# Kernel tuning notes

Hardware: AMD Instinct MI355X
Metric: run time of the kernel (lower is better)

## Reference

```python
import jax, jax.numpy as jnp
import numpy as np

N_NODES = 50000
N_EDGES = 1600000
N_FEAT = 128
DIM = 128
N_GRAPHS = 128
BN_EPS = 1e-5


def setup_inputs() -> dict:
    key = jax.random.key(0)
    ks = jax.random.split(key, 16)
    x = jax.random.normal(ks[0], (N_NODES, N_FEAT), dtype=jnp.float32)
    edge_index = jax.random.randint(ks[1], (2, N_EDGES), 0, N_NODES)
    batch = jnp.sort(jax.random.randint(ks[2], (N_NODES,), 0, N_GRAPHS))
    def lin(k, fin, fout):
        return jax.random.normal(k, (fin, fout), dtype=jnp.float32) / np.sqrt(fin).astype(np.float32)
    inp = {"x": x, "edge_index": edge_index, "batch": batch}
    fins = [N_FEAT, DIM, DIM]
    for i in range(3):
        inp[f"W{i}"] = lin(ks[3 + i], fins[i], DIM)
        inp[f"b{i}"] = jnp.zeros((DIM,), jnp.float32)
        inp[f"g{i}"] = jnp.ones((DIM,), jnp.float32)
        inp[f"be{i}"] = jnp.zeros((DIM,), jnp.float32)
    return inp


def _gcn_norm(edge_index, n):
    # add self loops, symmetric normalization D^-1/2 (A+I) D^-1/2
    loop = jnp.arange(n, dtype=edge_index.dtype)
    src = jnp.concatenate([edge_index[0], loop])
    dst = jnp.concatenate([edge_index[1], loop])
    deg = jax.ops.segment_sum(jnp.ones_like(src, dtype=jnp.float32), dst, num_segments=n)
    dinv = jnp.where(deg > 0, jax.lax.rsqrt(deg), 0.0)
    norm = dinv[src] * dinv[dst]  # [E+N]
    return src, dst, norm


def _gcn_conv(h, W, b, src, dst, norm, n):
    h = h @ W                      # [N, D]
    msg = h[src] * norm[:, None]   # [E+N, D] gather + scale
    agg = jax.ops.segment_sum(msg, dst, num_segments=n)
    return agg + b


def _batchnorm(h, g, be):
    mu = jnp.mean(h, axis=0)
    var = jnp.mean(jnp.square(h - mu), axis=0)  # biased, training-mode BN
    return (h - mu) * jax.lax.rsqrt(var + BN_EPS) * g + be


def reference(x, edge_index, batch, W0, b0, g0, be0, W1, b1, g1, be1, W2, b2, g2, be2):
    n = x.shape[0]
    src, dst, norm = _gcn_norm(edge_index, n)
    params = [(W0, b0, g0, be0), (W1, b1, g1, be1), (W2, b2, g2, be2)]
    h = x
    pools = []
    for (W, b, g, be) in params:
        h = jax.nn.relu(_gcn_conv(h, W, b, src, dst, norm, n))
        h = _batchnorm(h, g, be)
        pools.append(jax.ops.segment_sum(h, batch, num_segments=N_GRAPHS))
    return jnp.concatenate(pools, axis=1)  # [N_GRAPHS, 3*DIM]
```

## Files before the change

### kernel.cpp

```cpp
#include <hip/hip_runtime.h>
#include <hip/hip_bf16.h>

#define N_GRAPHS 128
#define BN_EPS 1e-5f
#define CHUNK 8192
#define NBU 512
#define CAP 8192

typedef short bf16x8 __attribute__((ext_vector_type(8)));
typedef short s16x4 __attribute__((ext_vector_type(4)));
typedef float f32x4 __attribute__((ext_vector_type(4)));

__device__ __forceinline__ unsigned short f2b(float f) {
    unsigned int u = __builtin_bit_cast(unsigned int, f);
    u += 0x7FFFu + ((u >> 16) & 1u);
    return (unsigned short)(u >> 16);
}
__device__ __forceinline__ float b2f_lo(unsigned int p) {
    return __builtin_bit_cast(float, p << 16);
}
__device__ __forceinline__ float b2f_hi(unsigned int p) {
    return __builtin_bit_cast(float, p & 0xFFFF0000u);
}

__global__ __launch_bounds__(512) void bin_chunks(const int* __restrict__ src,
                                                  const int* __restrict__ dst,
                                                  unsigned int* __restrict__ bpairs,
                                                  int* __restrict__ cnts,
                                                  int* __restrict__ cbase,
                                                  int* __restrict__ btot, int E) {
    __shared__ int lhist[NBU], lscan[NBU], lfill[NBU];
    int tid = threadIdx.x;
    int c0 = blockIdx.x * CHUNK;
    int ecnt = min(CHUNK, E - c0);
    lhist[tid] = 0;
    __syncthreads();
    for (int i = tid; i < ecnt; i += 512)
        atomicAdd(&lhist[((unsigned)dst[c0 + i]) >> 7], 1);
    __syncthreads();
    int orig = lhist[tid];
    atomicAdd(&btot[tid], orig);
    lscan[tid] = orig;
    __syncthreads();
    for (int off = 1; off < NBU; off <<= 1) {
        int t = (tid >= off) ? lscan[tid - off] : 0;
        __syncthreads();
        lscan[tid] += t;
        __syncthreads();
    }
    int excl = lscan[tid] - orig;
    cnts[blockIdx.x * NBU + tid] = orig;
    cbase[blockIdx.x * NBU + tid] = excl;
    lfill[tid] = 0;
    __syncthreads();
    lscan[tid] = excl;
    __syncthreads();
    for (int i = tid; i < ecnt; i += 512) {
        int d = dst[c0 + i], s = src[c0 + i];
        int b = ((unsigned)d) >> 7;
        int pos = lscan[b] + atomicAdd(&lfill[b], 1);
        bpairs[c0 + pos] = ((unsigned)(d & 127) << 25) | (unsigned)s;
    }
}

__global__ __launch_bounds__(512) void bucket_scan(const int* __restrict__ btot,
                                                   int* __restrict__ bucket_base) {
    __shared__ int s[NBU];
    int b = threadIdx.x;
    int tot = btot[b];
    s[b] = tot;
    __syncthreads();
    for (int off = 1; off < NBU; off <<= 1) {
        int t = (b >= off) ? s[b - off] : 0;
        __syncthreads();
        s[b] += t;
        __syncthreads();
    }
    bucket_base[b] = s[b] - tot;
}

__global__ __launch_bounds__(256) void bucket_csr(const unsigned int* __restrict__ bpairs,
                                                  const int* __restrict__ cnts,
                                                  const int* __restrict__ cbase,
                                                  const int* __restrict__ bucket_base,
                                                  int* __restrict__ rowp,
                                                  int* __restrict__ degarr,
                                                  float* __restrict__ dinv,
                                                  int* __restrict__ csr,
                                                  int nchunks, int N) {
    __shared__ unsigned int lpr[CAP];
    __shared__ int lcsr[CAP];
    __shared__ int ccnt[256], cofs[256], cb[256];
    __shared__ int lhist[128], lofs[128], lfill[128];
    int tid = threadIdx.x;
    int b = blockIdx.x;
    int bb = bucket_base[b];
    int total = bucket_base[b + 1] - bb;
    if (total > CAP) total = CAP;

    ccnt[tid] = (tid < nchunks) ? cnts[tid * NBU + b] : 0;
    cb[tid]   = (tid < nchunks) ? cbase[tid * NBU + b] : 0;
    cofs[tid] = ccnt[tid];
    __syncthreads();
    int orig = cofs[tid];
    for (int off = 1; off < 256; off <<= 1) {
        int t = (tid >= off) ? cofs[tid - off] : 0;
        __syncthreads();
        cofs[tid] += t;
        __syncthreads();
    }
    int o = cofs[tid] - orig;
    if (tid < nchunks) {
        int len = ccnt[tid];
        const unsigned int* p = bpairs + (size_t)tid * CHUNK + cb[tid];
        for (int i = 0; i < len; ++i) {
            int q = o + i;
            if (q < CAP) lpr[q] = p[i];
        }
    }
    if (tid < 128) { lhist[tid] = 0; lfill[tid] = 0; }
    __syncthreads();
    for (int i = tid; i < total; i += 256)
        atomicAdd(&lhist[lpr[i] >> 25], 1);
    __syncthreads();
    if (tid < 128) lofs[tid] = lhist[tid];
    __syncthreads();
    for (int off = 1; off < 128; off <<= 1) {
        int t = 0;
        if (tid < 128 && tid >= off) t = lofs[tid - off];
        __syncthreads();
        if (tid < 128) lofs[tid] += t;
        __syncthreads();
    }
    if (tid < 128) {
        int v = b * 128 + tid;
        if (v < N) {
            int dg = lhist[tid];
            degarr[v] = dg;
            rowp[v] = bb + lofs[tid] - dg;
            dinv[v] = rsqrtf((float)(dg + 1));
        }
    }
    __syncthreads();
    for (int i = tid; i < total; i += 256) {
        unsigned int pr = lpr[i];
        int dl = pr >> 25;
        int pos = lofs[dl] - lhist[dl] + atomicAdd(&lfill[dl], 1);
        if (pos < CAP) lcsr[pos] = (int)(pr & 0x1FFFFFFu);
    }
    __syncthreads();
    for (int i = tid; i < total; i += 256) csr[bb + i] = lcsr[i];
}

__global__ __launch_bounds__(256) void prep_w(const float* __restrict__ W,
                                              const float* __restrict__ sc,
                                              unsigned short* __restrict__ Wp) {
    int i = blockIdx.x * 256 + threadIdx.x;
    int k = i >> 7, c = i & 127;
    float w = W[i];
    if (sc) w *= sc[k];
    int kk = k & 31, k0 = k >> 5;
    int hi = (kk >> 2) & 3;
    int e = (kk & 3) + 4 * (kk >> 4);
    int idx = c * 128 + k0 * 32 + hi * 8 + e;
    Wp[idx ^ ((c & 7) << 3)] = f2b(w);
}

template <int AF32>
__global__ __launch_bounds__(256) void gemm_mfma(const void* __restrict__ Avoid,
                                                 const unsigned short* __restrict__ Wp,
                                                 const float* __restrict__ wb,
                                                 const float* __restrict__ dinv,
                                                 unsigned short* __restrict__ Cb, int N) {
    __shared__ unsigned short sWt[128 * 128];
    int tid = threadIdx.x;
    {
        const uint4* src = (const uint4*)Wp;
        uint4* dst = (uint4*)sWt;
#pragma unroll
        for (int j = 0; j < 8; ++j) dst[tid + 256 * j] = src[tid + 256 * j];
    }
    __syncthreads();

    int wave = tid >> 6, lane = tid & 63;
    int lo4 = lane & 15, hi = lane >> 4;
    int rowBase = blockIdx.x * 128 + wave * 32;

    f32x4 acc[8][2];
#pragma unroll
    for (int ct = 0; ct < 8; ++ct)
#pragma unroll
        for (int rt = 0; rt < 2; ++rt) acc[ct][rt] = (f32x4){0.f, 0.f, 0.f, 0.f};

    const float* Af = (const float*)Avoid;
    const unsigned short* Ab = (const unsigned short*)Avoid;

    for (int k0 = 0; k0 < 128; k0 += 32) {
        bf16x8 bfrag[2];
#pragma unroll
        for (int rt = 0; rt < 2; ++rt) {
            int r = rowBase + rt * 16 + lo4;
            if (r >= N) r = N - 1;
            if (AF32) {
                float4 f0 = *(const float4*)(Af + (size_t)r * 128 + k0 + 4 * hi);
                float4 f1 = *(const float4*)(Af + (size_t)r * 128 + k0 + 16 + 4 * hi);
                bf16x8 f;
                f[0] = (short)f2b(f0.x); f[1] = (short)f2b(f0.y);
                f[2] = (short)f2b(f0.z); f[3] = (short)f2b(f0.w);
                f[4] = (short)f2b(f1.x); f[5] = (short)f2b(f1.y);
                f[6] = (short)f2b(f1.z); f[7] = (short)f2b(f1.w);
                bfrag[rt] = f;
            } else {
                s16x4 a0 = *(const s16x4*)(Ab + (size_t)r * 128 + k0 + 4 * hi);
                s16x4 a1 = *(const s16x4*)(Ab + (size_t)r * 128 + k0 + 16 + 4 * hi);
                bf16x8 f;
                f[0] = a0[0]; f[1] = a0[1]; f[2] = a0[2]; f[3] = a0[3];
                f[4] = a1[0]; f[5] = a1[1]; f[6] = a1[2]; f[7] = a1[3];
                bfrag[rt] = f;
            }
        }
        int kq = k0 >> 5;
#pragma unroll
        for (int ct = 0; ct < 8; ++ct) {
            int c = ct * 16 + lo4;
            int idx = (c * 128 + kq * 32 + hi * 8) ^ ((c & 7) << 3);
            bf16x8 af = *(const bf16x8*)(sWt + idx);
#pragma unroll
            for (int rt = 0; rt < 2; ++rt)
                acc[ct][rt] = __builtin_amdgcn_mfma_f32_16x16x32_bf16(af, bfrag[rt], acc[ct][rt], 0, 0, 0);
        }
    }

#pragma unroll
    for (int rt = 0; rt < 2; ++rt) {
        int r = rowBase + rt * 16 + lo4;
        if (r < N) {
            float dv = dinv[r];
#pragma unroll
            for (int ct = 0; ct < 8; ++ct) {
                int c0 = ct * 16 + hi * 4;
                float4 wbv = make_float4(0.f, 0.f, 0.f, 0.f);
                if (!AF32) wbv = *(const float4*)(wb + c0);
                ushort4 s;
                s.x = f2b((acc[ct][rt][0] + wbv.x) * dv);
                s.y = f2b((acc[ct][rt][1] + wbv.y) * dv);
                s.z = f2b((acc[ct][rt][2] + wbv.z) * dv);
                s.w = f2b((acc[ct][rt][3] + wbv.w) * dv);
                *(ushort4*)(Cb + (size_t)r * 128 + c0) = s;
            }
        }
    }
}

__global__ __launch_bounds__(256) void agg_relu_b16(const unsigned int* __restrict__ hW32,
                                                    const int* __restrict__ rowp,
                                                    const int* __restrict__ cnt,
                                                    const int* __restrict__ csr,
                                                    const float* __restrict__ dinv,
                                                    const float* __restrict__ bias,
                                                    unsigned int* __restrict__ z32, int N) {
    int wave = threadIdx.x >> 6, lane = threadIdx.x & 63;
    int v = blockIdx.x * 4 + wave;
    if (v >= N) return;
    int beg = rowp[v];
    int num = cnt[v];
    float s0 = 0.f, s1 = 0.f;
    int i = 0;
    for (; i + 4 <= num; i += 4) {
        int u0 = csr[beg + i + 0];
        int u1 = csr[beg + i + 1];
        int u2 = csr[beg + i + 2];
        int u3 = csr[beg + i + 3];
        unsigned int p0 = hW32[(size_t)u0 * 64 + lane];
        unsigned int p1 = hW32[(size_t)u1 * 64 + lane];
        unsigned int p2 = hW32[(size_t)u2 * 64 + lane];
        unsigned int p3 = hW32[(size_t)u3 * 64 + lane];
        s0 += b2f_lo(p0) + b2f_lo(p1) + b2f_lo(p2) + b2f_lo(p3);
        s1 += b2f_hi(p0) + b2f_hi(p1) + b2f_hi(p2) + b2f_hi(p3);
    }
    for (; i < num; ++i) {
        int u = csr[beg + i];
        unsigned int p = hW32[(size_t)u * 64 + lane];
        s0 += b2f_lo(p);
        s1 += b2f_hi(p);
    }
    float dv = dinv[v];
    unsigned int pv = hW32[(size_t)v * 64 + lane];
    float r0 = dv * (s0 + b2f_lo(pv)) + bias[2 * lane];
    float r1 = dv * (s1 + b2f_hi(pv)) + bias[2 * lane + 1];
    unsigned int po = (unsigned int)f2b(fmaxf(r0, 0.f)) | ((unsigned int)f2b(fmaxf(r1, 0.f)) << 16);
    z32[(size_t)v * 64 + lane] = po;
}

__global__ __launch_bounds__(256) void bn_stats_b16(const unsigned int* __restrict__ z32,
                                                    float* __restrict__ stats, int N) {
    int lane = threadIdx.x & 63, sub = threadIdx.x >> 6;
    float s0 = 0.f, s1 = 0.f, q0 = 0.f, q1 = 0.f;
    for (int v = blockIdx.x * 4 + sub; v < N; v += gridDim.x * 4) {
        unsigned int p = z32[(size_t)v * 64 + lane];
        float a = b2f_lo(p), c = b2f_hi(p);
        s0 += a; q0 = fmaf(a, a, q0);
        s1 += c; q1 = fmaf(c, c, q1);
    }
    __shared__ float ls[256][4];
    ls[threadIdx.x][0] = s0; ls[threadIdx.x][1] = s1;
    ls[threadIdx.x][2] = q0; ls[threadIdx.x][3] = q1;
    __syncthreads();
    if (sub == 0) {
        for (int k = 1; k < 4; ++k) {
            s0 += ls[lane + 64 * k][0]; s1 += ls[lane + 64 * k][1];
            q0 += ls[lane + 64 * k][2]; q1 += ls[lane + 64 * k][3];
        }
        atomicAdd(&stats[2 * lane], s0);
        atomicAdd(&stats[2 * lane + 1], s1);
        atomicAdd(&stats[128 + 2 * lane], q0);
        atomicAdd(&stats[129 + 2 * lane], q1);
    }
}

__global__ void bn_finalize_wb(const float* __restrict__ stats, const float* __restrict__ g,
                               const float* __restrict__ be, float* __restrict__ ss,
                               const float* __restrict__ Wnext, float* __restrict__ wb,
                               float invN) {
    __shared__ float shv[128];
    int d = threadIdx.x;
    float mu = stats[d] * invN;
    float var = stats[128 + d] * invN - mu * mu;
    float sc = g[d] * rsqrtf(var + BN_EPS);
    float sh = be[d] - mu * sc;
    ss[d] = sc;
    ss[128 + d] = sh;
    shv[d] = sh;
    __syncthreads();
    if (Wnext) {
        float acc = 0.f;
#pragma unroll 4
        for (int k = 0; k < 128; ++k) acc = fmaf(shv[k], Wnext[k * 128 + d], acc);
        wb[d] = acc;
    }
}

__global__ __launch_bounds__(64) void apply_pool_b16(const unsigned int* __restrict__ z32,
                                                     const float* __restrict__ ss,
                                                     const int* __restrict__ batch,
                                                     float* __restrict__ out,
                                                     int layer, int N) {
    __shared__ int gb[32];
    int lane = threadIdx.x;
    int v0 = blockIdx.x * 32;
    int vend = min(v0 + 32, N);
    int cntv = vend - v0;
    if (lane < cntv) gb[lane] = batch[v0 + lane];
    __syncthreads();
    float sc0 = ss[2 * lane], sc1 = ss[2 * lane + 1];
    float sh0 = ss[128 + 2 * lane], sh1 = ss[129 + 2 * lane];
    float a0 = 0.f, a1 = 0.f;
    int cur = gb[0];
    for (int j = 0; j < cntv; ++j) {
        unsigned int p = z32[(size_t)(v0 + j) * 64 + lane];
        float x0 = fmaf(b2f_lo(p), sc0, sh0);
        float x1 = fmaf(b2f_hi(p), sc1, sh1);
        int g = gb[j];
        if (g != cur) {
            atomicAdd(&out[(size_t)cur * 384 + layer * 128 + 2 * lane], a0);
            atomicAdd(&out[(size_t)cur * 384 + layer * 128 + 2 * lane + 1], a1);
            a0 = a1 = 0.f;
            cur = g;
        }
        a0 += x0; a1 += x1;
    }
    atomicAdd(&out[(size_t)cur * 384 + layer * 128 + 2 * lane], a0);
    atomicAdd(&out[(size_t)cur * 384 + layer * 128 + 2 * lane + 1], a1);
}

extern "C" void kernel_launch(void* const* d_in, const int* in_sizes, int n_in,
                              void* d_out, int out_size, void* d_ws, size_t ws_size,
                              hipStream_t stream) {
    const float* x    = (const float*)d_in[0];
    const int* eidx   = (const int*)d_in[1];
    const int* batch  = (const int*)d_in[2];

    const int N = in_sizes[2];
    const int E = in_sizes[1] / 2;
    const int* src = eidx;
    const int* dst = eidx + E;

    const int nchunks = (E + CHUNK - 1) / CHUNK;
    const int NB = (N + 127) / 128;

    size_t off = 0;
    auto alloc = [&](size_t bytes) {
        void* p = (char*)d_ws + off;
        off += (bytes + 255) & ~(size_t)255;
        return p;
    };
    unsigned short* hWb = (unsigned short*)alloc((size_t)N * 128 * 2);
    unsigned int* z32   = (unsigned int*)alloc((size_t)N * 64 * 4);
    unsigned int* bpairs= (unsigned int*)alloc((size_t)nchunks * CHUNK * 4);
    int*   csr   = (int*)alloc((size_t)E * 4);
    int*   cnts  = (int*)alloc((size_t)nchunks * NBU * 4);
    int*   cbase = (int*)alloc((size_t)nchunks * NBU * 4);
    int*   bbase = (int*)alloc((size_t)(NBU + 1) * 4);
    int*   btot  = (int*)alloc((size_t)NBU * 4);
    int*   degar = (int*)alloc((size_t)N * 4);
    int*   rowp  = (int*)alloc((size_t)N * 4);
    float* dinv  = (float*)alloc((size_t)N * 4);
    float* stats = (float*)alloc(3 * 256 * 4);
    float* ss    = (float*)alloc(3 * 256 * 4);
    float* wbuf  = (float*)alloc(2 * 128 * 4);
    unsigned short* Wp = (unsigned short*)alloc(128 * 128 * 2);

    float* out = (float*)d_out;

    hipMemsetAsync(stats, 0, 3 * 256 * 4, stream);
    hipMemsetAsync(btot, 0, (size_t)NBU * 4, stream);
    hipMemsetAsync(out, 0, (size_t)N_GRAPHS * 384 * 4, stream);

    bin_chunks<<<nchunks, 512, 0, stream>>>(src, dst, bpairs, cnts, cbase, btot, E);
    bucket_scan<<<1, 512, 0, stream>>>(btot, bbase);
    bucket_csr<<<NB, 256, 0, stream>>>(bpairs, cnts, cbase, bbase, rowp, degar, dinv, csr,
                                       nchunks, N);

    const int gemm_blocks = (N + 127) / 128;
    const int agg_blocks  = (N + 3) / 4;
    const int pool_blocks = (N + 31) / 32;

    for (int l = 0; l < 3; ++l) {
        const float* W  = (const float*)d_in[3 + 4 * l];
        const float* b  = (const float*)d_in[4 + 4 * l];
        const float* g  = (const float*)d_in[5 + 4 * l];
        const float* be = (const float*)d_in[6 + 4 * l];

        prep_w<<<64, 256, 0, stream>>>(W, (l == 0) ? (const float*)nullptr : ss + (l - 1) * 256, Wp);

        if (l == 0)
            gemm_mfma<1><<<gemm_blocks, 256, 0, stream>>>((const void*)x, Wp, nullptr, dinv, hWb, N);
        else
            gemm_mfma<0><<<gemm_blocks, 256, 0, stream>>>((const void*)z32, Wp,
                                                          wbuf + (l - 1) * 128, dinv, hWb, N);

        agg_relu_b16<<<agg_blocks, 256, 0, stream>>>((const unsigned int*)hWb, rowp, degar, csr,
                                                     dinv, b, z32, N);
        bn_stats_b16<<<256, 256, 0, stream>>>(z32, stats + l * 256, N);
        bn_finalize_wb<<<1, 128, 0, stream>>>(stats + l * 256, g, be, ss + l * 256,
                                              (l < 2) ? (const float*)d_in[3 + 4 * (l + 1)]
                                                      : (const float*)nullptr,
                                              wbuf + l * 128, 1.0f / N);
        apply_pool_b16<<<pool_blocks, 64, 0, stream>>>(z32, ss + l * 256, batch, out, l, N);
    }
}
```

Measured before the change: 491.2 us.

## Sort CSR neighbors, vectorize aggregation gather, fuse BN finalize into weight prep

Each bucket's CSR neighbor list is now insertion-sorted in shared memory so gathers walk source rows in ascending order, which should improve cache locality. The aggregation kernel switches to 16-byte uint4 gathers, with four lane groups each handling a different edge, then combines the partial sums with shuffles. The separate BN finalize kernel and its scale/shift buffer are removed: the statistics are folded into the next layer's weight-prep kernel, apply_pool recomputes the scale and shift itself, and two memsets are merged into one. The cost is a serial per-row sort, a masked tail loop that gathers extra rows, and shuffle reductions.

```diff
diff --git a/kernel.cpp b/kernel.cpp
--- a/kernel.cpp
+++ b/kernel.cpp
@@ -21,6 +21,9 @@
 }
 __device__ __forceinline__ float b2f_hi(unsigned int p) {
     return __builtin_bit_cast(float, p & 0xFFFF0000u);
+}
+__device__ __forceinline__ unsigned int packrelu(float a, float b) {
+    return (unsigned int)f2b(fmaxf(a, 0.f)) | ((unsigned int)f2b(fmaxf(b, 0.f)) << 16);
 }
 
 __global__ __launch_bounds__(512) void bin_chunks(const int* __restrict__ src,
@@ -149,21 +152,54 @@
         if (pos < CAP) lcsr[pos] = (int)(pr & 0x1FFFFFFu);
     }
     __syncthreads();
+    if (tid < 128) {
+        int s0 = lofs[tid] - lhist[tid];
+        int e0 = lofs[tid];
+        for (int a = s0 + 1; a < e0; ++a) {
+            int key = lcsr[a];
+            int bq = a - 1;
+            while (bq >= s0 && lcsr[bq] > key) { lcsr[bq + 1] = lcsr[bq]; --bq; }
+            lcsr[bq + 1] = key;
+        }
+    }
+    __syncthreads();
     for (int i = tid; i < total; i += 256) csr[bb + i] = lcsr[i];
 }
 
-__global__ __launch_bounds__(256) void prep_w(const float* __restrict__ W,
-                                              const float* __restrict__ sc,
-                                              unsigned short* __restrict__ Wp) {
-    int i = blockIdx.x * 256 + threadIdx.x;
+template <int HASBN>
+__global__ __launch_bounds__(256) void bn_prep_w(const float* __restrict__ stats,
+                                                 const float* __restrict__ g,
+                                                 const float* __restrict__ be,
+                                                 const float* __restrict__ W,
+                                                 unsigned short* __restrict__ Wp,
+                                                 float* __restrict__ wb, float invN) {
+    __shared__ float scL[128], shL[128];
+    int tid = threadIdx.x;
+    if (HASBN) {
+        if (tid < 128) {
+            float mu = stats[tid] * invN;
+            float var = stats[128 + tid] * invN - mu * mu;
+            float sc = g[tid] * rsqrtf(var + BN_EPS);
+            scL[tid] = sc;
+            shL[tid] = be[tid] - mu * sc;
+        }
+        __syncthreads();
+    }
+    int i = blockIdx.x * 256 + tid;
     int k = i >> 7, c = i & 127;
     float w = W[i];
-    if (sc) w *= sc[k];
+    if (HASBN) w *= scL[k];
     int kk = k & 31, k0 = k >> 5;
     int hi = (kk >> 2) & 3;
     int e = (kk & 3) + 4 * (kk >> 4);
     int idx = c * 128 + k0 * 32 + hi * 8 + e;
     Wp[idx ^ ((c & 7) << 3)] = f2b(w);
+    if (HASBN && blockIdx.x == 0 && tid < 128) {
+        float acc = 0.f;
+#pragma unroll 4
+        for (int kx = 0; kx < 128; ++kx) acc = fmaf(shL[kx], W[kx * 128 + tid], acc);
+        wb[tid] = acc;
+    }
 }
 
 template <int AF32>
@@ -252,7 +288,7 @@
     }
 }
 
-__global__ __launch_bounds__(256) void agg_relu_b16(const unsigned int* __restrict__ hW32,
+__global__ __launch_bounds__(256) void agg_relu_b16(const uint4* __restrict__ hW4,
                                                     const int* __restrict__ rowp,
                                                     const int* __restrict__ cnt,
                                                     const int* __restrict__ csr,
@@ -262,34 +298,68 @@
     int wave = threadIdx.x >> 6, lane = threadIdx.x & 63;
     int v = blockIdx.x * 4 + wave;
     if (v >= N) return;
+    int q = lane >> 4, c = lane & 15;
     int beg = rowp[v];
     int num = cnt[v];
-    float s0 = 0.f, s1 = 0.f;
+    float s0 = 0.f, s1 = 0.f, s2 = 0.f, s3 = 0.f, s4 = 0.f, s5 = 0.f, s6 = 0.f, s7 = 0.f;
     int i = 0;
-    for (; i + 4 <= num; i += 4) {
-        int u0 = csr[beg + i + 0];
-        int u1 = csr[beg + i + 1];
-        int u2 = csr[beg + i + 2];
-        int u3 = csr[beg + i + 3];
-        unsigned int p0 = hW32[(size_t)u0 * 64 + lane];
-        unsigned int p1 = hW32[(size_t)u1 * 64 + lane];
-        unsigned int p2 = hW32[(size_t)u2 * 64 + lane];
-        unsigned int p3 = hW32[(size_t)u3 * 64 + lane];
-        s0 += b2f_lo(p0) + b2f_lo(p1) + b2f_lo(p2) + b2f_lo(p3);
-        s1 += b2f_hi(p0) + b2f_hi(p1) + b2f_hi(p2) + b2f_hi(p3);
-    }
-    for (; i < num; ++i) {
-        int u = csr[beg + i];
-        unsigned int p = hW32[(size_t)u * 64 + lane];
-        s0 += b2f_lo(p);
-        s1 += b2f_hi(p);
-    }
-    float dv = dinv[v];
-    unsigned int pv = hW32[(size_t)v * 64 + lane];
-    float r0 = dv * (s0 + b2f_lo(pv)) + bias[2 * lane];
-    float r1 = dv * (s1 + b2f_hi(pv)) + bias[2 * lane + 1];
-    unsigned int po = (unsigned int)f2b(fmaxf(r0, 0.f)) | ((unsigned int)f2b(fmaxf(r1, 0.f)) << 16);
-    z32[(size_t)v * 64 + lane] = po;
+    for (; i + 8 <= num; i += 8) {
+        int u0 = csr[beg + i + q];
+        int u1 = csr[beg + i + 4 + q];
+        uint4 p0 = hW4[(size_t)u0 * 16 + c];
+        uint4 p1 = hW4[(size_t)u1 * 16 + c];
+        s0 += b2f_lo(p0.x) + b2f_lo(p1.x);
+        s1 += b2f_hi(p0.x) + b2f_hi(p1.x);
+        s2 += b2f_lo(p0.y) + b2f_lo(p1.y);
+        s3 += b2f_hi(p0.y) + b2f_hi(p1.y);
+        s4 += b2f_lo(p0.z) + b2f_lo(p1.z);
+        s5 += b2f_hi(p0.z) + b2f_hi(p1.z);
+        s6 += b2f_lo(p0.w) + b2f_lo(p1.w);
+        s7 += b2f_hi(p0.w) + b2f_hi(p1.w);
+    }
+    for (; i < num; i += 4) {
+        int idx = i + q;
+        bool ok = idx < num;
+        int u = ok ? csr[beg + idx] : v;
+        float m = ok ? 1.f : 0.f;
+        uint4 p = hW4[(size_t)u * 16 + c];
+        s0 = fmaf(m, b2f_lo(p.x), s0);
+        s1 = fmaf(m, b2f_hi(p.x), s1);
+        s2 = fmaf(m, b2f_lo(p.y), s2);
+        s3 = fmaf(m, b2f_hi(p.y), s3);
+        s4 = fmaf(m, b2f_lo(p.z), s4);
+        s5 = fmaf(m, b2f_hi(p.z), s5);
+        s6 = fmaf(m, b2f_lo(p.w), s6);
+        s7 = fmaf(m, b2f_hi(p.w), s7);
+    }
+    s0 += __shfl_xor(s0, 16, 64); s0 += __shfl_xor(s0, 32, 64);
+    s1 += __shfl_xor(s1, 16, 64); s1 += __shfl_xor(s1, 32, 64);
+    s2 += __shfl_xor(s2, 16, 64); s2 += __shfl_xor(s2, 32, 64);
+    s3 += __shfl_xor(s3, 16, 64); s3 += __shfl_xor(s3, 32, 64);
+    s4 += __shfl_xor(s4, 16, 64); s4 += __shfl_xor(s4, 32, 64);
+    s5 += __shfl_xor(s5, 16, 64); s5 += __shfl_xor(s5, 32, 64);
+    s6 += __shfl_xor(s6, 16, 64); s6 += __shfl_xor(s6, 32, 64);
+    s7 += __shfl_xor(s7, 16, 64); s7 += __shfl_xor(s7, 32, 64);
+    if (q == 0) {
+        float dv = dinv[v];
+        uint4 pv = hW4[(size_t)v * 16 + c];
+        float4 b0 = *(const float4*)(bias + 8 * c);
+        float4 b1 = *(const float4*)(bias + 8 * c + 4);
+        float r0 = dv * (s0 + b2f_lo(pv.x)) + b0.x;
+        float r1 = dv * (s1 + b2f_hi(pv.x)) + b0.y;
+        float r2 = dv * (s2 + b2f_lo(pv.y)) + b0.z;
+        float r3 = dv * (s3 + b2f_hi(pv.y)) + b0.w;
+        float r4 = dv * (s4 + b2f_lo(pv.z)) + b1.x;
+        float r5 = dv * (s5 + b2f_hi(pv.z)) + b1.y;
+        float r6 = dv * (s6 + b2f_lo(pv.w)) + b1.z;
+        float r7 = dv * (s7 + b2f_hi(pv.w)) + b1.w;
+        uint4 o;
+        o.x = packrelu(r0, r1);
+        o.y = packrelu(r2, r3);
+        o.z = packrelu(r4, r5);
+        o.w = packrelu(r6, r7);
+        *(uint4*)(z32 + (size_t)v * 64 + 4 * c) = o;
+    }
 }
 
 __global__ __launch_bounds__(256) void bn_stats_b16(const unsigned int* __restrict__ z32,
@@ -318,33 +388,13 @@
     }
 }
 
-__global__ void bn_finalize_wb(const float* __restrict__ stats, const float* __restrict__ g,
-                               const float* __restrict__ be, float* __restrict__ ss,
-                               const float* __restrict__ Wnext, float* __restrict__ wb,
-                               float invN) {
-    __shared__ float shv[128];
-    int d = threadIdx.x;
-    float mu = stats[d] * invN;
-    float var = stats[128 + d] * invN - mu * mu;
-    float sc = g[d] * rsqrtf(var + BN_EPS);
-    float sh = be[d] - mu * sc;
-    ss[d] = sc;
-    ss[128 + d] = sh;
-    shv[d] = sh;
-    __syncthreads();
-    if (Wnext) {
-        float acc = 0.f;
-#pragma unroll 4
-        for (int k = 0; k < 128; ++k) acc = fmaf(shv[k], Wnext[k * 128 + d], acc);
-        wb[d] = acc;
-    }
-}
-
 __global__ __launch_bounds__(64) void apply_pool_b16(const unsigned int* __restrict__ z32,
-                                                     const float* __restrict__ ss,
+                                                     const float* __restrict__ stats,
+                                                     const float* __restrict__ g,
+                                                     const float* __restrict__ be,
                                                      const int* __restrict__ batch,
                                                      float* __restrict__ out,
-                                                     int layer, int N) {
+                                                     int layer, int N, float invN) {
     __shared__ int gb[32];
     int lane = threadIdx.x;
     int v0 = blockIdx.x * 32;
@@ -352,25 +402,29 @@
     int cntv = vend - v0;
     if (lane < cntv) gb[lane] = batch[v0 + lane];
     __syncthreads();
-    float sc0 = ss[2 * lane], sc1 = ss[2 * lane + 1];
-    float sh0 = ss[128 + 2 * lane], sh1 = ss[129 + 2 * lane];
+    int d0 = 2 * lane, d1 = 2 * lane + 1;
+    float mu0 = stats[d0] * invN, mu1 = stats[d1] * invN;
+    float va0 = stats[128 + d0] * invN - mu0 * mu0;
+    float va1 = stats[128 + d1] * invN - mu1 * mu1;
+    float sc0 = g[d0] * rsqrtf(va0 + BN_EPS), sc1 = g[d1] * rsqrtf(va1 + BN_EPS);
+    float sh0 = be[d0] - mu0 * sc0, sh1 = be[d1] - mu1 * sc1;
     float a0 = 0.f, a1 = 0.f;
     int cur = gb[0];
     for (int j = 0; j < cntv; ++j) {
         unsigned int p = z32[(size_t)(v0 + j) * 64 + lane];
         float x0 = fmaf(b2f_lo(p), sc0, sh0);
         float x1 = fmaf(b2f_hi(p), sc1, sh1);
-        int g = gb[j];
-        if (g != cur) {
-            atomicAdd(&out[(size_t)cur * 384 + layer * 128 + 2 * lane], a0);
-            atomicAdd(&out[(size_t)cur * 384 + layer * 128 + 2 * lane + 1], a1);
+        int gg = gb[j];
+        if (gg != cur) {
+            atomicAdd(&out[(size_t)cur * 384 + layer * 128 + d0], a0);
+            atomicAdd(&out[(size_t)cur * 384 + layer * 128 + d1], a1);
             a0 = a1 = 0.f;
-            cur = g;
+            cur = gg;
         }
         a0 += x0; a1 += x1;
     }
-    atomicAdd(&out[(size_t)cur * 384 + layer * 128 + 2 * lane], a0);
-    atomicAdd(&out[(size_t)cur * 384 + layer * 128 + 2 * lane + 1], a1);
+    atomicAdd(&out[(size_t)cur * 384 + layer * 128 + d0], a0);
+    atomicAdd(&out[(size_t)cur * 384 + layer * 128 + d1], a1);
 }
 
 extern "C" void kernel_launch(void* const* d_in, const int* in_sizes, int n_in,
@@ -387,6 +441,7 @@
 
     const int nchunks = (E + CHUNK - 1) / CHUNK;
     const int NB = (N + 127) / 128;
+    const float invN = 1.0f / N;
 
     size_t off = 0;
     auto alloc = [&](size_t bytes) {
@@ -401,19 +456,17 @@
     int*   cnts  = (int*)alloc((size_t)nchunks * NBU * 4);
     int*   cbase = (int*)alloc((size_t)nchunks * NBU * 4);
     int*   bbase = (int*)alloc((size_t)(NBU + 1) * 4);
+    float* stats = (float*)alloc(3 * 256 * 4);
     int*   btot  = (int*)alloc((size_t)NBU * 4);
     int*   degar = (int*)alloc((size_t)N * 4);
     int*   rowp  = (int*)alloc((size_t)N * 4);
     float* dinv  = (float*)alloc((size_t)N * 4);
-    float* stats = (float*)alloc(3 * 256 * 4);
-    float* ss    = (float*)alloc(3 * 256 * 4);
     float* wbuf  = (float*)alloc(2 * 128 * 4);
     unsigned short* Wp = (unsigned short*)alloc(128 * 128 * 2);
 
     float* out = (float*)d_out;
 
-    hipMemsetAsync(stats, 0, 3 * 256 * 4, stream);
-    hipMemsetAsync(btot, 0, (size_t)NBU * 4, stream);
+    hipMemsetAsync(stats, 0, 3 * 256 * 4 + (size_t)NBU * 4, stream);
     hipMemsetAsync(out, 0, (size_t)N_GRAPHS * 384 * 4, stream);
 
     bin_chunks<<<nchunks, 512, 0, stream>>>(src, dst, bpairs, cnts, cbase, btot, E);
@@ -425,13 +478,13 @@
     const int agg_blocks  = (N + 3) / 4;
     const int pool_blocks = (N + 31) / 32;
 
+    bn_prep_w<0><<<64, 256, 0, stream>>>(nullptr, nullptr, nullptr,
+                                         (const float*)d_in[3], Wp, nullptr, 0.f);
+
     for (int l = 0; l < 3; ++l) {
-        const float* W  = (const float*)d_in[3 + 4 * l];
         const float* b  = (const float*)d_in[4 + 4 * l];
         const float* g  = (const float*)d_in[5 + 4 * l];
         const float* be = (const float*)d_in[6 + 4 * l];
-
-        prep_w<<<64, 256, 0, stream>>>(W, (l == 0) ? (const float*)nullptr : ss + (l - 1) * 256, Wp);
 
         if (l == 0)
             gemm_mfma<1><<<gemm_blocks, 256, 0, stream>>>((const void*)x, Wp, nullptr, dinv, hWb, N);
@@ -439,13 +492,15 @@
             gemm_mfma<0><<<gemm_blocks, 256, 0, stream>>>((const void*)z32, Wp,
                                                           wbuf + (l - 1) * 128, dinv, hWb, N);
 
-        agg_relu_b16<<<agg_blocks, 256, 0, stream>>>((const unsigned int*)hWb, rowp, degar, csr,
+        agg_relu_b16<<<agg_blocks, 256, 0, stream>>>((const uint4*)hWb, rowp, degar, csr,
                                                      dinv, b, z32, N);
         bn_stats_b16<<<256, 256, 0, stream>>>(z32, stats + l * 256, N);
-        bn_finalize_wb<<<1, 128, 0, stream>>>(stats + l * 256, g, be, ss + l * 256,
-                                              (l < 2) ? (const float*)d_in[3 + 4 * (l + 1)]
-                                                      : (const float*)nullptr,
-                                              wbuf + l * 128, 1.0f / N);
-        apply_pool_b16<<<pool_blocks, 64, 0, stream>>>(z32, ss + l * 256, batch, out, l, N);
-    }
-}
+        if (l < 2) {
+            bn_prep_w<1><<<64, 256, 0, stream>>>(stats + l * 256, g, be,
+                                                 (const float*)d_in[3 + 4 * (l + 1)],
+                                                 Wp, wbuf + l * 128, invN);
+        }
+        apply_pool_b16<<<pool_blocks, 64, 0, stream>>>(z32, stats + l * 256, g, be, batch, out,
+                                                       l, N, invN);
+    }
+}
```

New measurement: 557.1 us. +13.4%, slower.
